# Performance work log

Measured on AMD Instinct MI355X. Metric: run time of the kernel, lower is better.

The kernel has to match this reference:

```python
import jax, jax.numpy as jnp
import numpy as np

N_NODES = 50000
N_EDGES = 1500000
D = 512
LN_EPS = 1e-5


def setup_inputs() -> dict:
    key = jax.random.key(0)
    ks = jax.random.split(key, 8)
    scale = 1.0 / np.sqrt(D)
    return {
        "node_feature": jax.random.normal(ks[0], (N_NODES, D), dtype=jnp.float32),
        "edge_index": jax.random.randint(ks[1], (2, N_EDGES), 0, N_NODES, dtype=jnp.int32),
        "W_l": jax.random.uniform(ks[2], (D, D), jnp.float32, -scale, scale),  # neighbor lin
        "b_l": jnp.zeros((D,), jnp.float32),
        "W_r": jax.random.uniform(ks[3], (D, D), jnp.float32, -scale, scale),  # root lin (no bias)
        "gamma": jnp.ones((D,), jnp.float32),
        "beta": jnp.zeros((D,), jnp.float32),
    }


def _layer_norm(x, gamma, beta):
    mu = jnp.mean(x, axis=-1, keepdims=True)
    var = jnp.mean(jnp.square(x - mu), axis=-1, keepdims=True)
    return (x - mu) * jax.lax.rsqrt(var + LN_EPS) * gamma + beta


def reference(node_feature, edge_index, W_l, b_l, W_r, gamma, beta):
    n = node_feature.shape[0]
    residual = node_feature
    h = _layer_norm(node_feature, gamma, beta)
    src, dst = edge_index[0], edge_index[1]
    # mean-aggregate source features at destinations (gather + segment scatter)
    summed = jax.ops.segment_sum(h[src], dst, num_segments=n)  # [N, D]
    cnt = jax.ops.segment_sum(jnp.ones((src.shape[0],), h.dtype), dst, num_segments=n)
    mean = summed / jnp.maximum(cnt, 1.0)[:, None]
    # SAGEConv: lin_l(aggregated) + lin_r(root); bias on lin_l
    out = mean @ W_l.T + b_l + h @ W_r.T
    out = jax.nn.relu(out)
    return out + residual
```

## Files before the change

### kernel.cpp

```cpp
#include <hip/hip_runtime.h>


#define D_DIM 512

typedef __bf16 bf16x8 __attribute__((ext_vector_type(8)));
typedef float f32x4 __attribute__((ext_vector_type(4)));
typedef float f32x2 __attribute__((ext_vector_type(2)));

__device__ __forceinline__ unsigned short f2bf(float f) {
  unsigned u = __float_as_uint(f);
  u += 0x7fffu + ((u >> 16) & 1u);
  return (unsigned short)(u >> 16);
}
__device__ __forceinline__ float bflo(unsigned u) { return __uint_as_float(u << 16); }
__device__ __forceinline__ float bfhi(unsigned u) { return __uint_as_float(u & 0xffff0000u); }
__device__ __forceinline__ unsigned packbf2(float lo, float hi) {
  return (unsigned)f2bf(lo) | ((unsigned)f2bf(hi) << 16);
}

__global__ void ln_kernel(const float* __restrict__ x, const float* __restrict__ gamma,
                          const float* __restrict__ beta, unsigned short* __restrict__ Acat,
                          unsigned char* __restrict__ h8, int n, int use_fp8) {
  int lane = threadIdx.x & 63;
  int row = blockIdx.x * 4 + (threadIdx.x >> 6);
  if (row >= n) return;
  const float* xr = x + (size_t)row * D_DIM + lane * 8;
  float4 a = *(const float4*)xr;
  float4 b = *(const float4*)(xr + 4);
  float sum = a.x + a.y + a.z + a.w + b.x + b.y + b.z + b.w;
  float sq = a.x * a.x + a.y * a.y + a.z * a.z + a.w * a.w +
             b.x * b.x + b.y * b.y + b.z * b.z + b.w * b.w;
#pragma unroll
  for (int m = 1; m < 64; m <<= 1) {
    sum += __shfl_xor(sum, m, 64);
    sq  += __shfl_xor(sq, m, 64);
  }
  float mu = sum * (1.0f / D_DIM);
  float var = sq * (1.0f / D_DIM) - mu * mu;
  float rs = rsqrtf(var + 1e-5f);
  const float* gp = gamma + lane * 8;
  const float* bp = beta + lane * 8;
  float4 g0 = *(const float4*)gp, g1 = *(const float4*)(gp + 4);
  float4 e0 = *(const float4*)bp, e1 = *(const float4*)(bp + 4);
  float h0 = (a.x - mu) * rs * g0.x + e0.x;
  float h1 = (a.y - mu) * rs * g0.y + e0.y;
  float h2 = (a.z - mu) * rs * g0.z + e0.z;
  float h3 = (a.w - mu) * rs * g0.w + e0.w;
  float h4 = (b.x - mu) * rs * g1.x + e1.x;
  float h5 = (b.y - mu) * rs * g1.y + e1.y;
  float h6 = (b.z - mu) * rs * g1.z + e1.z;
  float h7 = (b.w - mu) * rs * g1.w + e1.w;
  uint4 st = { packbf2(h0, h1), packbf2(h2, h3), packbf2(h4, h5), packbf2(h6, h7) };
  *(uint4*)(Acat + (size_t)row * 1024 + 512 + lane * 8) = st;
  if (use_fp8) {
    int p0 = __builtin_amdgcn_cvt_pk_fp8_f32(h0, h1, 0, false);
    p0 = __builtin_amdgcn_cvt_pk_fp8_f32(h2, h3, p0, true);
    int p1 = __builtin_amdgcn_cvt_pk_fp8_f32(h4, h5, 0, false);
    p1 = __builtin_amdgcn_cvt_pk_fp8_f32(h6, h7, p1, true);
    uint2 st2 = { (unsigned)p0, (unsigned)p1 };
    *(uint2*)(h8 + (size_t)row * 512 + lane * 8) = st2;
  }
}

__global__ void wconv_kernel(const float* __restrict__ Wl, const float* __restrict__ Wr,
                             unsigned short* __restrict__ Wcat) {
  int id = blockIdx.x * 256 + threadIdx.x;
  int j = id >> 9, k = id & 511;
  Wcat[(size_t)j * 1024 + k] = f2bf(Wl[id]);
  Wcat[(size_t)j * 1024 + 512 + k] = f2bf(Wr[id]);
}

__global__ void zero_kernel(int* __restrict__ p, int n) {
  int i = blockIdx.x * 256 + threadIdx.x;
  if (i < n) p[i] = 0;
}

__global__ void hist_kernel(const int* __restrict__ dst, int nE, int* __restrict__ cnt) {
  int e = blockIdx.x * 256 + threadIdx.x;
  if (e < nE) atomicAdd(&cnt[dst[e]], 1);
}

__global__ void scan1_kernel(const int* __restrict__ cnt, int n,
                             int* __restrict__ excl, int* __restrict__ bsums) {
  __shared__ int wsum[16];
  int gid = blockIdx.x * 1024 + threadIdx.x;
  int lane = threadIdx.x & 63, wave = threadIdx.x >> 6;
  int v = (gid < n) ? cnt[gid] : 0;
  int s = v;
#pragma unroll
  for (int d = 1; d < 64; d <<= 1) {
    int t = __shfl_up(s, d, 64);
    if (lane >= d) s += t;
  }
  if (lane == 63) wsum[wave] = s;
  __syncthreads();
  if (wave == 0) {
    int ws = (lane < 16) ? wsum[lane] : 0;
#pragma unroll
    for (int d = 1; d < 16; d <<= 1) {
      int t = __shfl_up(ws, d, 64);
      if (lane >= d) ws += t;
    }
    if (lane < 16) wsum[lane] = ws;
  }
  __syncthreads();
  int incl = s + ((wave > 0) ? wsum[wave - 1] : 0);
  if (gid < n) excl[gid] = incl - v;
  if (threadIdx.x == 1023) bsums[blockIdx.x] = incl;
}

__global__ void scan2_kernel(int* __restrict__ bsums, int nb) {
  int lane = threadIdx.x;
  int v = (lane < nb) ? bsums[lane] : 0;
  int s = v;
#pragma unroll
  for (int d = 1; d < 64; d <<= 1) {
    int t = __shfl_up(s, d, 64);
    if (lane >= d) s += t;
  }
  if (lane < nb) bsums[lane] = s - v;
}

__global__ void scan3_kernel(int* __restrict__ rowst, int* __restrict__ cur,
                             const int* __restrict__ bsums, int n, int nE) {
  int gid = blockIdx.x * 1024 + threadIdx.x;
  if (gid < n) {
    int r = rowst[gid] + bsums[blockIdx.x];
    rowst[gid] = r;
    cur[gid] = r;
  }
  if (gid == 0) rowst[n] = nE;
}

__global__ void scatter_kernel(const int* __restrict__ src, const int* __restrict__ dst,
                               int nE, int* __restrict__ cur, int* __restrict__ sorted_src) {
  int e = blockIdx.x * 256 + threadIdx.x;
  if (e < nE) {
    int p = atomicAdd(&cur[dst[e]], 1);
    sorted_src[p] = src[e];
  }
}

__device__ __forceinline__ void acc_bf(float* acc, uint4 r) {
  acc[0] += bflo(r.x); acc[1] += bfhi(r.x);
  acc[2] += bflo(r.y); acc[3] += bfhi(r.y);
  acc[4] += bflo(r.z); acc[5] += bfhi(r.z);
  acc[6] += bflo(r.w); acc[7] += bfhi(r.w);
}

__device__ __forceinline__ void acc_f8(float* acc, uint2 r) {
  f32x2 a = __builtin_amdgcn_cvt_pk_f32_fp8(r.x, false);
  f32x2 b = __builtin_amdgcn_cvt_pk_f32_fp8(r.x, true);
  f32x2 c = __builtin_amdgcn_cvt_pk_f32_fp8(r.y, false);
  f32x2 d = __builtin_amdgcn_cvt_pk_f32_fp8(r.y, true);
  acc[0] += a.x; acc[1] += a.y; acc[2] += b.x; acc[3] += b.y;
  acc[4] += c.x; acc[5] += c.y; acc[6] += d.x; acc[7] += d.y;
}

__global__ void agg_kernel(unsigned short* __restrict__ Acat,
                           const unsigned char* __restrict__ h8,
                           const int* __restrict__ rowst,
                           const int* __restrict__ sorted_src, int n, int use_fp8) {
  int lane = threadIdx.x & 63;
  int node = blockIdx.x * 4 + (threadIdx.x >> 6);
  if (node >= n) return;
  int s0 = rowst[node], s1 = rowst[node + 1];
  float acc[8] = {0.f, 0.f, 0.f, 0.f, 0.f, 0.f, 0.f, 0.f};
  if (use_fp8) {
    const unsigned char* hb = h8 + lane * 8;
    int e = s0;
    for (; e + 3 < s1; e += 4) {
      int i0 = sorted_src[e], i1 = sorted_src[e + 1];
      int i2 = sorted_src[e + 2], i3 = sorted_src[e + 3];
      uint2 r0 = *(const uint2*)(hb + (size_t)i0 * 512);
      uint2 r1 = *(const uint2*)(hb + (size_t)i1 * 512);
      uint2 r2 = *(const uint2*)(hb + (size_t)i2 * 512);
      uint2 r3 = *(const uint2*)(hb + (size_t)i3 * 512);
      acc_f8(acc, r0); acc_f8(acc, r1); acc_f8(acc, r2); acc_f8(acc, r3);
    }
    for (; e < s1; ++e) {
      uint2 r0 = *(const uint2*)(hb + (size_t)sorted_src[e] * 512);
      acc_f8(acc, r0);
    }
  } else {
    const unsigned short* hbase = Acat + 512 + lane * 8;
    int e = s0;
    for (; e + 3 < s1; e += 4) {
      int i0 = sorted_src[e], i1 = sorted_src[e + 1];
      int i2 = sorted_src[e + 2], i3 = sorted_src[e + 3];
      uint4 r0 = *(const uint4*)(hbase + (size_t)i0 * 1024);
      uint4 r1 = *(const uint4*)(hbase + (size_t)i1 * 1024);
      uint4 r2 = *(const uint4*)(hbase + (size_t)i2 * 1024);
      uint4 r3 = *(const uint4*)(hbase + (size_t)i3 * 1024);
      acc_bf(acc, r0); acc_bf(acc, r1); acc_bf(acc, r2); acc_bf(acc, r3);
    }
    for (; e < s1; ++e) {
      uint4 r0 = *(const uint4*)(hbase + (size_t)sorted_src[e] * 1024);
      acc_bf(acc, r0);
    }
  }
  int deg = s1 - s0;
  float sc = (deg > 0) ? (1.0f / (float)deg) : 0.0f;
  uint4 st = { packbf2(acc[0] * sc, acc[1] * sc), packbf2(acc[2] * sc, acc[3] * sc),
               packbf2(acc[4] * sc, acc[5] * sc), packbf2(acc[6] * sc, acc[7] * sc) };
  *(uint4*)(Acat + (size_t)node * 1024 + lane * 8) = st;
}

__device__ __forceinline__ void async16(const unsigned short* g, char* lds) {
  __builtin_amdgcn_global_load_lds((const __attribute__((address_space(1))) void*)g,
                                   (__attribute__((address_space(3))) void*)lds, 16, 0, 0);
}

__global__ __launch_bounds__(256) void gemm_kernel(
    const unsigned short* __restrict__ A,
    const unsigned short* __restrict__ B,
    const float* __restrict__ bias,
    const float* __restrict__ residual,
    float* __restrict__ out, int M, int Mblocks) {
  __shared__ unsigned short sA[2][4096];
  __shared__ unsigned short sB[2][4096];
  const int K = 1024;
  int t = threadIdx.x;
  int lane = t & 63, wave = t >> 6;
  int quad = lane >> 4, l16 = lane & 15;
  int b = blockIdx.x;
  int mb = (b >> 5) * 8 + (b & 7);
  int nb = (b >> 3) & 3;
  if (mb >= Mblocks) return;
  int mBase = mb * 128, nBase = nb * 128;
  int wm = (wave & 1) * 64, wn = (wave >> 1) * 64;

  const unsigned short* gA = A + (size_t)(mBase + (t >> 2)) * K + (t & 3) * 8;
  const unsigned short* gB = B + (size_t)(nBase + (t >> 2)) * K + (t & 3) * 8;

  f32x4 acc[4][4] = {};

  auto issue = [&](int ks, int buf) {
    char* a0 = (char*)&sA[buf][0] + wave * 1024;
    char* b0 = (char*)&sB[buf][0] + wave * 1024;
    async16(gA + ks, a0);
    async16(gA + (size_t)64 * K + ks, a0 + 4096);
    async16(gB + ks, b0);
    async16(gB + (size_t)64 * K + ks, b0 + 4096);
  };
  auto compute = [&](int buf) {
    const unsigned short* pA = &sA[buf][0];
    const unsigned short* pB = &sB[buf][0];
    bf16x8 af[4], bfr[4];
#pragma unroll
    for (int i = 0; i < 4; ++i)
      af[i] = *(const bf16x8*)(pA + (wm + i * 16 + l16) * 32 + quad * 8);
#pragma unroll
    for (int j = 0; j < 4; ++j)
      bfr[j] = *(const bf16x8*)(pB + (wn + j * 16 + l16) * 32 + quad * 8);
#pragma unroll
    for (int i = 0; i < 4; ++i)
#pragma unroll
      for (int j = 0; j < 4; ++j)
        acc[i][j] = __builtin_amdgcn_mfma_f32_16x16x32_bf16(af[i], bfr[j], acc[i][j], 0, 0, 0);
  };

  issue(0, 0);
  for (int r = 0; r < 31; ++r) {
    int cur = r & 1;
    issue((r + 1) << 5, cur ^ 1);
    asm volatile("s_waitcnt vmcnt(4)\n\ts_barrier" ::: "memory");
    compute(cur);
    asm volatile("s_barrier" ::: "memory");
  }
  asm volatile("s_waitcnt vmcnt(0)\n\ts_barrier" ::: "memory");
  compute(1);

  float biasv[4];
#pragma unroll
  for (int j = 0; j < 4; ++j) biasv[j] = bias[nBase + wn + j * 16 + l16];
#pragma unroll
  for (int i = 0; i < 4; ++i) {
    int gr0 = mBase + wm + i * 16 + quad * 4;
#pragma unroll
    for (int j = 0; j < 4; ++j) {
      int col = nBase + wn + j * 16 + l16;
#pragma unroll
      for (int r = 0; r < 4; ++r) {
        int gr = gr0 + r;
        if (gr < M) {
          size_t idx = (size_t)gr * D_DIM + col;
          float v = acc[i][j][r] + biasv[j];
          float rv = __builtin_nontemporal_load(&residual[idx]);
          __builtin_nontemporal_store(fmaxf(v, 0.0f) + rv, &out[idx]);
        }
      }
    }
  }
}

extern "C" void kernel_launch(void* const* d_in, const int* in_sizes, int n_in,
                              void* d_out, int out_size, void* d_ws, size_t ws_size,
                              hipStream_t stream) {
  const float* x = (const float*)d_in[0];
  const int* ei = (const int*)d_in[1];
  const float* Wl = (const float*)d_in[2];
  const float* bl = (const float*)d_in[3];
  const float* Wr = (const float*)d_in[4];
  const float* gamma = (const float*)d_in[5];
  const float* beta = (const float*)d_in[6];
  float* out = (float*)d_out;

  int n = in_sizes[0] / D_DIM;
  int nE = in_sizes[1] / 2;
  const int* src = ei;
  const int* dstv = ei + nE;
  int Mpad = (n + 127) & ~127;
  int Mblocks = Mpad / 128;

  char* w = (char*)d_ws;
  size_t off = 0;
  auto carve = [&](size_t bytes) {
    char* p = w + off;
    off += (bytes + 255) & ~(size_t)255;
    return p;
  };
  unsigned short* Acat = (unsigned short*)carve((size_t)Mpad * 1024 * 2);
  unsigned short* Wcat = (unsigned short*)carve((size_t)512 * 1024 * 2);
  int* sorted = (int*)carve((size_t)nE * 4);
  int* cnt = (int*)carve((size_t)n * 4);
  int* rowst = (int*)carve((size_t)(n + 1) * 4);
  int* bsums = (int*)carve(1024);
  if (off > ws_size) return;

  size_t h8_bytes = (size_t)n * 512;
  int use_fp8 = (off + h8_bytes <= ws_size) ? 1 : 0;
  unsigned char* h8 = use_fp8 ? (unsigned char*)carve(h8_bytes) : (unsigned char*)w;

  int nbScan = (n + 1023) / 1024;

  ln_kernel<<<(n + 3) / 4, 256, 0, stream>>>(x, gamma, beta, Acat, h8, n, use_fp8);
  wconv_kernel<<<(512 * 512) / 256, 256, 0, stream>>>(Wl, Wr, Wcat);
  zero_kernel<<<(n + 255) / 256, 256, 0, stream>>>(cnt, n);
  hist_kernel<<<(nE + 255) / 256, 256, 0, stream>>>(dstv, nE, cnt);
  scan1_kernel<<<nbScan, 1024, 0, stream>>>(cnt, n, rowst, bsums);
  scan2_kernel<<<1, 64, 0, stream>>>(bsums, nbScan);
  scan3_kernel<<<nbScan, 1024, 0, stream>>>(rowst, cnt, bsums, n, nE);
  scatter_kernel<<<(nE + 255) / 256, 256, 0, stream>>>(src, dstv, nE, cnt, sorted);
  agg_kernel<<<(n + 3) / 4, 256, 0, stream>>>(Acat, h8, rowst, sorted, n, use_fp8);
  int gemmBlocks = ((Mblocks + 7) / 8) * 32;
  gemm_kernel<<<gemmBlocks, 256, 0, stream>>>(Acat, Wcat, bl, x, out, n, Mblocks);
}
```

Before: 652.3 us.

## Enlarge GEMM tile to 256x128 with 8 waves, K=64 stages and XOR-swizzled LDS

The fused-concat GEMM now runs 512-thread blocks computing 256x128 output tiles with a 64-wide K step, half as many barrier rounds. LDS tiles are XOR-swizzled by row to avoid bank conflicts on the fragment reads. MFMA sections get raised wave priority via s_setprio. The goal is more reuse per global load and less sync overhead, at the cost of 96KB of LDS per block, fewer blocks overall, and a prefetch that waits on vmcnt(0) each step.

After: 670.6 us. 1.03x slower.

```diff
diff --git a/kernel.cpp b/kernel.cpp
--- a/kernel.cpp
+++ b/kernel.cpp
@@ -211,14 +211,14 @@
                                    (__attribute__((address_space(3))) void*)lds, 16, 0, 0);
 }
 
-__global__ __launch_bounds__(256) void gemm_kernel(
+__global__ __launch_bounds__(512, 2) void gemm_kernel(
     const unsigned short* __restrict__ A,
     const unsigned short* __restrict__ B,
     const float* __restrict__ bias,
     const float* __restrict__ residual,
-    float* __restrict__ out, int M, int Mblocks) {
-  __shared__ unsigned short sA[2][4096];
-  __shared__ unsigned short sB[2][4096];
+    float* __restrict__ out, int M, int Mtiles) {
+  __shared__ unsigned short sA[2][256 * 64];
+  __shared__ unsigned short sB[2][128 * 64];
   const int K = 1024;
   int t = threadIdx.x;
   int lane = t & 63, wave = t >> 6;
@@ -226,49 +226,66 @@
   int b = blockIdx.x;
   int mb = (b >> 5) * 8 + (b & 7);
   int nb = (b >> 3) & 3;
-  if (mb >= Mblocks) return;
-  int mBase = mb * 128, nBase = nb * 128;
-  int wm = (wave & 1) * 64, wn = (wave >> 1) * 64;
-
-  const unsigned short* gA = A + (size_t)(mBase + (t >> 2)) * K + (t & 3) * 8;
-  const unsigned short* gB = B + (size_t)(nBase + (t >> 2)) * K + (t & 3) * 8;
+  if (mb >= Mtiles) return;
+  int mBase = mb * 256, nBase = nb * 128;
+  int wm = (wave >> 1) * 64;
+  int wn = (wave & 1) * 64;
+
+  int srow = t >> 3;
+  int schunk = ((t & 7) ^ ((t >> 3) & 7)) * 8;
+  const unsigned short* gAb = A + (size_t)(mBase + srow) * K + schunk;
+  const unsigned short* gBb = B + (size_t)(nBase + srow) * K + schunk;
 
   f32x4 acc[4][4] = {};
 
-  auto issue = [&](int ks, int buf) {
-    char* a0 = (char*)&sA[buf][0] + wave * 1024;
-    char* b0 = (char*)&sB[buf][0] + wave * 1024;
-    async16(gA + ks, a0);
-    async16(gA + (size_t)64 * K + ks, a0 + 4096);
-    async16(gB + ks, b0);
-    async16(gB + (size_t)64 * K + ks, b0 + 4096);
+  auto stage = [&](int buf, int kt) {
+    int kOff = kt << 6;
+    char* la = (char*)&sA[buf][0] + wave * 1024;
+    char* lb = (char*)&sB[buf][0] + wave * 1024;
+#pragma unroll
+    for (int ia = 0; ia < 4; ++ia)
+      async16(gAb + (size_t)ia * 64 * K + kOff, la + ia * 8192);
+#pragma unroll
+    for (int ib = 0; ib < 2; ++ib)
+      async16(gBb + (size_t)ib * 64 * K + kOff, lb + ib * 8192);
   };
+
+  int swz = (l16 & 7);
   auto compute = [&](int buf) {
     const unsigned short* pA = &sA[buf][0];
     const unsigned short* pB = &sB[buf][0];
-    bf16x8 af[4], bfr[4];
-#pragma unroll
-    for (int i = 0; i < 4; ++i)
-      af[i] = *(const bf16x8*)(pA + (wm + i * 16 + l16) * 32 + quad * 8);
-#pragma unroll
-    for (int j = 0; j < 4; ++j)
-      bfr[j] = *(const bf16x8*)(pB + (wn + j * 16 + l16) * 32 + quad * 8);
-#pragma unroll
-    for (int i = 0; i < 4; ++i)
-#pragma unroll
-      for (int j = 0; j < 4; ++j)
-        acc[i][j] = __builtin_amdgcn_mfma_f32_16x16x32_bf16(af[i], bfr[j], acc[i][j], 0, 0, 0);
+#pragma unroll
+    for (int kk = 0; kk < 2; ++kk) {
+      bf16x8 af[4], bfr[4];
+#pragma unroll
+      for (int i = 0; i < 4; ++i) {
+        int rr = wm + i * 16 + l16;
+        int pc = (kk * 4 + quad) ^ swz;
+        af[i] = *(const bf16x8*)(pA + rr * 64 + pc * 8);
+      }
+#pragma unroll
+      for (int j = 0; j < 4; ++j) {
+        int rb = wn + j * 16 + l16;
+        int pc = (kk * 4 + quad) ^ swz;
+        bfr[j] = *(const bf16x8*)(pB + rb * 64 + pc * 8);
+      }
+      __builtin_amdgcn_s_setprio(1);
+#pragma unroll
+      for (int i = 0; i < 4; ++i)
+#pragma unroll
+        for (int j = 0; j < 4; ++j)
+          acc[i][j] = __builtin_amdgcn_mfma_f32_16x16x32_bf16(af[i], bfr[j], acc[i][j], 0, 0, 0);
+      __builtin_amdgcn_s_setprio(0);
+    }
   };
 
-  issue(0, 0);
-  for (int r = 0; r < 31; ++r) {
-    int cur = r & 1;
-    issue((r + 1) << 5, cur ^ 1);
-    asm volatile("s_waitcnt vmcnt(4)\n\ts_barrier" ::: "memory");
-    compute(cur);
-    asm volatile("s_barrier" ::: "memory");
-  }
+  stage(0, 0);
   asm volatile("s_waitcnt vmcnt(0)\n\ts_barrier" ::: "memory");
+  for (int kt = 0; kt < 15; ++kt) {
+    stage((kt + 1) & 1, kt + 1);
+    compute(kt & 1);
+    asm volatile("s_waitcnt vmcnt(0)\n\ts_barrier" ::: "memory");
+  }
   compute(1);
 
   float biasv[4];
@@ -310,8 +327,8 @@
   int nE = in_sizes[1] / 2;
   const int* src = ei;
   const int* dstv = ei + nE;
-  int Mpad = (n + 127) & ~127;
-  int Mblocks = Mpad / 128;
+  int Mpad = (n + 255) & ~255;
+  int Mtiles = Mpad / 256;
 
   char* w = (char*)d_ws;
   size_t off = 0;
@@ -343,6 +360,6 @@
   scan3_kernel<<<nbScan, 1024, 0, stream>>>(rowst, cnt, bsums, n, nE);
   scatter_kernel<<<(nE + 255) / 256, 256, 0, stream>>>(src, dstv, nE, cnt, sorted);
   agg_kernel<<<(n + 3) / 4, 256, 0, stream>>>(Acat, h8, rowst, sorted, n, use_fp8);
-  int gemmBlocks = ((Mblocks + 7) / 8) * 32;
-  gemm_kernel<<<gemmBlocks, 256, 0, stream>>>(Acat, Wcat, bl, x, out, n, Mblocks);
-}
+  int gemmBlocks = ((Mtiles + 7) / 8) * 32;
+  gemm_kernel<<<gemmBlocks, 512, 0, stream>>>(Acat, Wcat, bl, x, out, n, Mtiles);
+}
```

## Retile GEMM to 64-row by full-512-column blocks with swizzled LDS

Applied to the files above, without the earlier changes.

The GEMM now gives each block 64 rows and all 512 output columns, with each wave owning 128 columns, in place of 128x128 tiles. The A tile (aggregated and LN features) is read from global memory only once instead of four times, while the weight matrix is re-streamed by every block. LDS chunks are XOR-swizzled to reduce bank conflicts, staging is deepened, s_setprio is placed around the MFMAs, and launch_bounds asks for two blocks per CU. The risks are more accumulator registers (32 f32x4 per thread), a larger LDS footprint, and more B traffic per output.

Measured after the change: 683.0 us. 4.7% more time.

```diff
diff --git a/kernel.cpp b/kernel.cpp
--- a/kernel.cpp
+++ b/kernel.cpp
@@ -211,75 +211,79 @@
                                    (__attribute__((address_space(3))) void*)lds, 16, 0, 0);
 }
 
-__global__ __launch_bounds__(256) void gemm_kernel(
+__global__ __launch_bounds__(256, 2) void gemm_kernel(
     const unsigned short* __restrict__ A,
     const unsigned short* __restrict__ B,
     const float* __restrict__ bias,
     const float* __restrict__ residual,
-    float* __restrict__ out, int M, int Mblocks) {
-  __shared__ unsigned short sA[2][4096];
-  __shared__ unsigned short sB[2][4096];
+    float* __restrict__ out, int M) {
+  __shared__ unsigned short sA[2][64 * 32];
+  __shared__ unsigned short sB[2][512 * 32];
   const int K = 1024;
   int t = threadIdx.x;
-  int lane = t & 63, wave = t >> 6;
+  int lane = t & 63;
   int quad = lane >> 4, l16 = lane & 15;
-  int b = blockIdx.x;
-  int mb = (b >> 5) * 8 + (b & 7);
-  int nb = (b >> 3) & 3;
-  if (mb >= Mblocks) return;
-  int mBase = mb * 128, nBase = nb * 128;
-  int wm = (wave & 1) * 64, wn = (wave >> 1) * 64;
-
-  const unsigned short* gA = A + (size_t)(mBase + (t >> 2)) * K + (t & 3) * 8;
-  const unsigned short* gB = B + (size_t)(nBase + (t >> 2)) * K + (t & 3) * 8;
-
-  f32x4 acc[4][4] = {};
-
-  auto issue = [&](int ks, int buf) {
-    char* a0 = (char*)&sA[buf][0] + wave * 1024;
-    char* b0 = (char*)&sB[buf][0] + wave * 1024;
-    async16(gA + ks, a0);
-    async16(gA + (size_t)64 * K + ks, a0 + 4096);
-    async16(gB + ks, b0);
-    async16(gB + (size_t)64 * K + ks, b0 + 4096);
+  int wv = t >> 6;
+  int mBase = blockIdx.x * 64;
+  int wn = wv * 128;
+
+  int srow = t >> 2;
+  int schunk = ((t & 3) ^ ((t >> 2) & 3)) * 8;
+  const unsigned short* gA = A + (size_t)(mBase + srow) * K + schunk;
+  const unsigned short* gB = B + (size_t)srow * K + schunk;
+
+  f32x4 acc[4][8] = {};
+
+  auto stage = [&](int buf, int kt) {
+    int kOff = kt << 5;
+    char* la = (char*)&sA[buf][0] + wv * 1024;
+    char* lb = (char*)&sB[buf][0] + wv * 1024;
+    async16(gA + kOff, la);
+#pragma unroll
+    for (int ib = 0; ib < 8; ++ib)
+      async16(gB + (size_t)ib * 64 * K + kOff, lb + ib * 4096);
   };
+
+  int swz = l16 & 3;
   auto compute = [&](int buf) {
-    const unsigned short* pA = &sA[buf][0];
-    const unsigned short* pB = &sB[buf][0];
-    bf16x8 af[4], bfr[4];
+    bf16x8 af[4], bfr[8];
 #pragma unroll
     for (int i = 0; i < 4; ++i)
-      af[i] = *(const bf16x8*)(pA + (wm + i * 16 + l16) * 32 + quad * 8);
-#pragma unroll
-    for (int j = 0; j < 4; ++j)
-      bfr[j] = *(const bf16x8*)(pB + (wn + j * 16 + l16) * 32 + quad * 8);
+      af[i] = *(const bf16x8*)(&sA[buf][(i * 16 + l16) * 32 + ((quad ^ swz) * 8)]);
+#pragma unroll
+    for (int j = 0; j < 8; ++j)
+      bfr[j] = *(const bf16x8*)(&sB[buf][(wn + j * 16 + l16) * 32 + ((quad ^ swz) * 8)]);
+    __builtin_amdgcn_s_setprio(1);
 #pragma unroll
     for (int i = 0; i < 4; ++i)
 #pragma unroll
-      for (int j = 0; j < 4; ++j)
+      for (int j = 0; j < 8; ++j)
         acc[i][j] = __builtin_amdgcn_mfma_f32_16x16x32_bf16(af[i], bfr[j], acc[i][j], 0, 0, 0);
+    __builtin_amdgcn_s_setprio(0);
   };
 
-  issue(0, 0);
-  for (int r = 0; r < 31; ++r) {
-    int cur = r & 1;
-    issue((r + 1) << 5, cur ^ 1);
-    asm volatile("s_waitcnt vmcnt(4)\n\ts_barrier" ::: "memory");
-    compute(cur);
+  stage(0, 0);
+  stage(1, 1);
+  for (int kt = 0; kt < 30; ++kt) {
+    asm volatile("s_waitcnt vmcnt(9)\n\ts_barrier" ::: "memory");
+    compute(kt & 1);
     asm volatile("s_barrier" ::: "memory");
-  }
+    stage(kt & 1, kt + 2);
+  }
+  asm volatile("s_waitcnt vmcnt(9)\n\ts_barrier" ::: "memory");
+  compute(0);
   asm volatile("s_waitcnt vmcnt(0)\n\ts_barrier" ::: "memory");
   compute(1);
 
-  float biasv[4];
-#pragma unroll
-  for (int j = 0; j < 4; ++j) biasv[j] = bias[nBase + wn + j * 16 + l16];
+  float biasv[8];
+#pragma unroll
+  for (int j = 0; j < 8; ++j) biasv[j] = bias[wn + j * 16 + l16];
 #pragma unroll
   for (int i = 0; i < 4; ++i) {
-    int gr0 = mBase + wm + i * 16 + quad * 4;
-#pragma unroll
-    for (int j = 0; j < 4; ++j) {
-      int col = nBase + wn + j * 16 + l16;
+    int gr0 = mBase + i * 16 + quad * 4;
+#pragma unroll
+    for (int j = 0; j < 8; ++j) {
+      int col = wn + j * 16 + l16;
 #pragma unroll
       for (int r = 0; r < 4; ++r) {
         int gr = gr0 + r;
@@ -310,8 +314,8 @@
   int nE = in_sizes[1] / 2;
   const int* src = ei;
   const int* dstv = ei + nE;
-  int Mpad = (n + 127) & ~127;
-  int Mblocks = Mpad / 128;
+  int Mpad = (n + 63) & ~63;
+  int Mtiles = Mpad / 64;
 
   char* w = (char*)d_ws;
   size_t off = 0;
@@ -343,6 +347,5 @@
   scan3_kernel<<<nbScan, 1024, 0, stream>>>(rowst, cnt, bsums, n, nE);
   scatter_kernel<<<(nE + 255) / 256, 256, 0, stream>>>(src, dstv, nE, cnt, sorted);
   agg_kernel<<<(n + 3) / 4, 256, 0, stream>>>(Acat, h8, rowst, sorted, n, use_fp8);
-  int gemmBlocks = ((Mblocks + 7) / 8) * 32;
-  gemm_kernel<<<gemmBlocks, 256, 0, stream>>>(Acat, Wcat, bl, x, out, n, Mblocks);
-}
+  gemm_kernel<<<Mtiles, 256, 0, stream>>>(Acat, Wcat, bl, x, out, n);
+}
```
